# Optimization experiments

Hardware: AMD Instinct MI355X
Metric: run time of the kernel (lower is better)

## Reference

```python
import jax, jax.numpy as jnp
import numpy as np

B, TK, NK, H = 64, 512, 256, 512

def _masked_renorm_softmax(scores, mask):
    # softmax over last dim, multiply by mask, renormalize (as in the torch code)
    p = jax.nn.softmax(scores, axis=-1) * mask
    return p / jnp.sum(p, axis=-1, keepdims=True)

def setup_inputs() -> dict:
    key = jax.random.key(0)
    ks = jax.random.split(key, 14)
    s = 0.02
    return {
        "s_t_hat": jax.random.normal(ks[0], (B, 2 * H), jnp.float32),
        "encoder_outputs_token": jax.random.normal(ks[1], (B, TK, H), jnp.float32),
        "encoder_outputs_node": jax.random.normal(ks[2], (B, NK, H), jnp.float32),
        "node_to_token": jax.random.randint(ks[3], (B, TK), 0, NK),
        "enc_padding_mask_token": jnp.ones((B, TK), jnp.float32),
        "enc_padding_mask_node": jnp.ones((B, NK), jnp.float32),
        "graph": jax.random.uniform(ks[4], (B, NK, NK), jnp.float32),
        "flow": jax.random.uniform(ks[5], (B, NK), jnp.float32),
        # parameters (Linear weights stored as [in, out]; x @ W == torch Linear)
        "W_c": jax.random.normal(ks[6], (H,), jnp.float32) * s,          # Linear(1, H)
        "W_tok": jax.random.normal(ks[7], (H, H), jnp.float32) * s,      # encode_proj_token
        "W_node": jax.random.normal(ks[8], (H, H), jnp.float32) * s,     # encode_proj_node
        "W_dec": jax.random.normal(ks[9], (2 * H, H), jnp.float32) * s,  # decode_proj
        "b_dec": jnp.zeros((H,), jnp.float32),
        "v_tok": jax.random.normal(ks[10], (H,), jnp.float32) * s,       # v_token
        "v_node": jax.random.normal(ks[11], (H,), jnp.float32) * s,      # v_node
    }

def reference(s_t_hat, encoder_outputs_token, encoder_outputs_node, node_to_token,
              enc_padding_mask_token, enc_padding_mask_node, graph, flow,
              W_c, W_tok, W_node, W_dec, b_dec, v_tok, v_node):
    # projections
    enc_tok_feat = jnp.einsum('bth,hk->btk', encoder_outputs_token, W_tok)   # [B,TK,H]
    enc_node_feat = jnp.einsum('bnh,hk->bnk', encoder_outputs_node, W_node)  # [B,NK,H]
    dec_fea = s_t_hat @ W_dec + b_dec                                        # [B,H]
    flow_feat = flow[..., None] * W_c                                        # [B,NK,H]

    # node attention
    e_node = jnp.tanh(enc_node_feat + dec_fea[:, None, :] + flow_feat)
    scores_node = jnp.einsum('bnh,h->bn', e_node, v_node)                    # [B,NK]
    attn_dist_node = _masked_renorm_softmax(scores_node, enc_padding_mask_node)

    # gather node attention onto tokens via node_to_token indices
    gathered = jnp.take_along_axis(attn_dist_node, node_to_token, axis=1)    # [B,TK]
    attn_dist_node_to_token = _masked_renorm_softmax(gathered, enc_padding_mask_token)

    # token attention
    e_tok = jnp.tanh(enc_tok_feat + dec_fea[:, None, :])
    scores_tok = jnp.einsum('bth,h->bt', e_tok, v_tok)                       # [B,TK]
    attn_dist_token = _masked_renorm_softmax(scores_tok, enc_padding_mask_token)

    # mix and context
    final_attn = 0.5 * attn_dist_token + 0.5 * attn_dist_node_to_token      # [B,TK]
    c_t = jnp.einsum('bt,bth->bh', final_attn, encoder_outputs_token)        # [B,H]

    # multi-hop graph diffusion of node attention
    zero_hop = attn_dist_node                                                # [B,NK]
    one_hop = jnp.einsum('bn,bnm->bm', zero_hop, graph)
    two_hop = jnp.einsum('bn,bnm->bm', one_hop, graph)
    flow_out = (zero_hop + one_hop + two_hop) * 0.33333

    return (c_t, final_attn, attn_dist_node, flow_out)
```

## Files before the change

### kernel.cpp

```cpp
#include <hip/hip_runtime.h>
#include <math.h>

constexpr int kB = 64;
constexpr int kTK = 512;
constexpr int kNK = 256;
constexpr int kH = 512;
constexpr int kTokBlocks = kB * kTK / 64;
constexpr int kNodeBlocks = kB * kNK / 64;

typedef float f32x4 __attribute__((ext_vector_type(4)));
typedef __bf16 bf16x8 __attribute__((ext_vector_type(8)));
typedef unsigned short u16x8 __attribute__((ext_vector_type(8)));

__device__ __forceinline__ unsigned short f32_to_bf16(float f) {
  return (unsigned short)((__float_as_uint(f) + 0x8000u) >> 16);
}

__device__ __forceinline__ float tanh_fast(float x) {
  float e = __builtin_amdgcn_exp2f(x * 2.8853900817779268f);
  return 1.0f - 2.0f * __builtin_amdgcn_rcpf(e + 1.0f);
}

__device__ __forceinline__ void lds_barrier() {
  __builtin_amdgcn_s_waitcnt(0xC07F);
  __builtin_amdgcn_s_barrier();
}

__global__ __launch_bounds__(256) void prep_kernel(
    const float* __restrict__ Wtok, const float* __restrict__ Wnode,
    unsigned short* __restrict__ WtokT, unsigned short* __restrict__ WnodeT,
    const float* __restrict__ s_t_hat, const float* __restrict__ W_dec,
    float* __restrict__ dec_part) {
  __shared__ float sm[32 * 33];
  const int tid = threadIdx.x;
  if (blockIdx.x < 512) {
    const int idx = blockIdx.x;
    const int z = idx >> 8, rem = idx & 255;
    const int bx = rem & 15, by = rem >> 4;
    const float* W = z ? Wnode : Wtok;
    unsigned short* T = z ? WnodeT : WtokT;
    const int tx = tid & 31, ty = tid >> 5;
#pragma unroll
    for (int i = 0; i < 4; ++i)
      sm[(ty + 8 * i) * 33 + tx] =
          W[(size_t)(by * 32 + ty + 8 * i) * kH + bx * 32 + tx];
    __syncthreads();
#pragma unroll
    for (int i = 0; i < 4; ++i)
      T[(size_t)(bx * 32 + ty + 8 * i) * kH + by * 32 + tx] =
          f32_to_bf16(sm[tx * 33 + ty + 8 * i]);
  } else {
    const int r = blockIdx.x - 512;
    const int b = r >> 3, s = r & 7;
    if (tid < 128) sm[tid] = s_t_hat[(size_t)b * 1024 + s * 128 + tid];
    __syncthreads();
    float a0 = 0.f, a1 = 0.f;
    const float* w = W_dec + (size_t)(s * 128) * kH;
#pragma unroll 8
    for (int k = 0; k < 128; ++k) {
      a0 = fmaf(sm[k], w[(size_t)k * kH + tid], a0);
      a1 = fmaf(sm[k], w[(size_t)k * kH + tid + 256], a1);
    }
    dec_part[(size_t)(b * 8 + s) * kH + tid] = a0;
    dec_part[(size_t)(b * 8 + s) * kH + tid + 256] = a1;
  }
}

__global__ __launch_bounds__(1024, 4) void scores_fused_kernel(
    const float* __restrict__ enc_tok, const float* __restrict__ enc_node,
    const unsigned short* __restrict__ WtokT,
    const unsigned short* __restrict__ WnodeT,
    const float* __restrict__ dec_part, const float* __restrict__ b_dec,
    const float* __restrict__ flow, const float* __restrict__ W_c,
    const float* __restrict__ v_tok, const float* __restrict__ v_node,
    float* __restrict__ scores_tok, float* __restrict__ scores_node) {
  const int tid = threadIdx.x;
  const int wave = tid >> 6, lane = tid & 63;
  const int quad = lane >> 4, l15 = lane & 15;
  const bool is_node = blockIdx.x >= kTokBlocks;
  const int bidx = is_node ? (int)blockIdx.x - kTokBlocks : (int)blockIdx.x;
  const float* A = is_node ? enc_node : enc_tok;
  const unsigned short* WT = is_node ? WnodeT : WtokT;
  const float* v = is_node ? v_node : v_tok;
  float* scores = is_node ? scores_node : scores_tok;
  const int ROWS = is_node ? kNK : kTK;
  const int b = is_node ? (bidx >> 2) : (bidx >> 3);
  const int row0 = (is_node ? (bidx & 3) : (bidx & 7)) * 64;

  __shared__ __align__(16) unsigned short As[2][8192];
  __shared__ float red[16][64];

  const f32x4 fzero = {0.f, 0.f, 0.f, 0.f};
  f32x4 acc[4][2];
#pragma unroll
  for (int i = 0; i < 4; ++i)
#pragma unroll
    for (int j = 0; j < 2; ++j) acc[i][j] = fzero;

  const int arow = ((tid >> 6) & 3) * 16 + (tid & 15);
  const int akk = (tid >> 8) * 32 + ((tid >> 4) & 3) * 8;
  const float* aptr = A + (size_t)(b * ROWS + row0 + arow) * kH + akk;
  float4 ax0, ax1;
  auto aload = [&](int kc) {
    ax0 = *(const float4*)(aptr + kc * 128);
    ax1 = *(const float4*)(aptr + kc * 128 + 4);
  };
  auto acommit = [&](int buf) {
    u16x8 h;
    h[0] = f32_to_bf16(ax0.x); h[1] = f32_to_bf16(ax0.y);
    h[2] = f32_to_bf16(ax0.z); h[3] = f32_to_bf16(ax0.w);
    h[4] = f32_to_bf16(ax1.x); h[5] = f32_to_bf16(ax1.y);
    h[6] = f32_to_bf16(ax1.z); h[7] = f32_to_bf16(ax1.w);
    *(u16x8*)&As[buf][tid * 8] = h;
  };

  const int n0 = wave * 32;
  const unsigned short* bbase = WT + (size_t)(n0 + l15) * kH + quad * 8;
  bf16x8 bbuf[2][2];
  auto loadB = [&](int sb, int g) {
    bbuf[sb][0] = *(const bf16x8*)(bbase + g * 32);
    bbuf[sb][1] = *(const bf16x8*)(bbase + (size_t)16 * kH + g * 32);
  };

  aload(0);
  acommit(0);
  aload(1);
  loadB(0, 0);
  lds_barrier();

#pragma unroll
  for (int g = 0; g < 16; ++g) {
    const int kc = g >> 2, kh = g & 3;
    if (kh == 0 && kc < 3) {
      acommit((kc + 1) & 1);
      if (kc < 2) aload(kc + 2);
    }
    if (g < 15) loadB((g + 1) & 1, g + 1);
    bf16x8 afr[4];
#pragma unroll
    for (int mi = 0; mi < 4; ++mi)
      afr[mi] = *(const bf16x8*)&As[kc & 1][((kh * 4 + mi) * 64 + lane) * 8];
#pragma unroll
    for (int mi = 0; mi < 4; ++mi)
#pragma unroll
      for (int ni = 0; ni < 2; ++ni)
        acc[mi][ni] = __builtin_amdgcn_mfma_f32_16x16x32_bf16(
            afr[mi], bbuf[g & 1][ni], acc[mi][ni], 0, 0, 0);
    if (kh == 3 && kc < 3) lds_barrier();
  }

  float dec2[2], vv2[2], wc2[2];
#pragma unroll
  for (int ni = 0; ni < 2; ++ni) {
    const int col = n0 + 16 * ni + l15;
    float d = b_dec[col];
#pragma unroll
    for (int p = 0; p < 8; ++p) d += dec_part[(size_t)(b * 8 + p) * kH + col];
    dec2[ni] = d;
    vv2[ni] = v[col];
    wc2[ni] = is_node ? W_c[col] : 0.f;
  }
#pragma unroll
  for (int mi = 0; mi < 4; ++mi) {
#pragma unroll
    for (int reg = 0; reg < 4; ++reg) {
      const int row = 16 * mi + quad * 4 + reg;
      const float fl = is_node ? flow[b * kNK + row0 + row] : 0.f;
      float p = 0.f;
#pragma unroll
      for (int ni = 0; ni < 2; ++ni)
        p += tanh_fast(fmaf(fl, wc2[ni], acc[mi][ni][reg] + dec2[ni])) * vv2[ni];
#pragma unroll
      for (int off = 1; off < 16; off <<= 1) p += __shfl_xor(p, off, 64);
      if (l15 == 0) red[wave][row] = p;
    }
  }
  __syncthreads();
  if (tid < 64) {
    float s = 0.f;
#pragma unroll
    for (int w = 0; w < 16; ++w) s += red[w][tid];
    scores[b * ROWS + row0 + tid] = s;
  }
}

__device__ __forceinline__ float block_sum_512(float v, float* rbuf) {
#pragma unroll
  for (int off = 32; off >= 1; off >>= 1) v += __shfl_xor(v, off, 64);
  if ((threadIdx.x & 63) == 0) rbuf[threadIdx.x >> 6] = v;
  __syncthreads();
  float s = rbuf[0];
#pragma unroll
  for (int w = 1; w < 8; ++w) s += rbuf[w];
  __syncthreads();
  return s;
}

__global__ __launch_bounds__(512) void softmax_mix_kernel(
    const float* __restrict__ scores_node, const float* __restrict__ scores_tok,
    const int* __restrict__ node_to_token,
    const float* __restrict__ mask_tok, const float* __restrict__ mask_node,
    float* __restrict__ out_final, float* __restrict__ out_attn_node,
    float* __restrict__ out_flow) {
  const int b = blockIdx.x, tid = threadIdx.x;
  __shared__ float an_sh[kNK];
  __shared__ float rbuf[8];

  if (tid < kNK) out_flow[b * kNK + tid] = 0.f;

  float en = 0.f;
  if (tid < kNK)
    en = expf(scores_node[b * kNK + tid]) * mask_node[b * kNK + tid];
  float sn = block_sum_512(en, rbuf);
  float an = en / sn;
  if (tid < kNK) {
    an_sh[tid] = an;
    out_attn_node[b * kNK + tid] = an;
  }
  __syncthreads();

  const float mt = mask_tok[b * kTK + tid];
  const int idx = node_to_token[b * kTK + tid];
  float eg = expf(an_sh[idx]) * mt;
  float sg = block_sum_512(eg, rbuf);
  float an2t = eg / sg;

  float et = expf(scores_tok[b * kTK + tid]) * mt;
  float st = block_sum_512(et, rbuf);
  float at = et / st;

  out_final[b * kTK + tid] = 0.5f * (at + an2t);
}

__global__ __launch_bounds__(512) void ct_flow1_kernel(
    const float* __restrict__ final_attn, const float* __restrict__ enc_tok,
    const float* __restrict__ attn_node, const float* __restrict__ graph,
    float* __restrict__ ctp, float* __restrict__ fp1) {
  __shared__ float sm[64];
  const int tid = threadIdx.x;
  if (blockIdx.x < 512) {
    const int s = blockIdx.x & 7, b = blockIdx.x >> 3;
    if (tid < 64) sm[tid] = final_attn[b * kTK + s * 64 + tid];
    __syncthreads();
    float acc = 0.f;
    const float* base = enc_tok + ((size_t)(b * kTK + s * 64)) * kH + tid;
#pragma unroll 16
    for (int t = 0; t < 64; ++t) acc = fmaf(sm[t], base[(size_t)t * kH], acc);
    ctp[(size_t)(b * 8 + s) * kH + tid] = acc;
  } else {
    const int r = blockIdx.x - 512;
    const int b = r >> 2, sl = r & 3;
    const int m = tid & 255, half = tid >> 8;
    if (tid < 64) sm[tid] = attn_node[b * kNK + sl * 64 + tid];
    __syncthreads();
    float acc = 0.f;
    const float* g =
        graph + ((size_t)(b * kNK + sl * 64 + half * 32)) * kNK + m;
#pragma unroll 8
    for (int n = 0; n < 32; ++n)
      acc = fmaf(sm[half * 32 + n], g[(size_t)n * kNK], acc);
    fp1[(size_t)(b * 8 + sl * 2 + half) * kNK + m] = acc;
  }
}

__global__ __launch_bounds__(512) void ct_flow2_kernel(
    const float* __restrict__ ctp, const float* __restrict__ fp1,
    const float* __restrict__ attn_node, const float* __restrict__ graph,
    float* __restrict__ out_ct, float* __restrict__ out_flow) {
  __shared__ float one_sh[64];
  const int tid = threadIdx.x;
  if (blockIdx.x < 64) {
    const int b = blockIdx.x;
    float acc = 0.f;
#pragma unroll
    for (int p = 0; p < 8; ++p) acc += ctp[(size_t)(b * 8 + p) * kH + tid];
    out_ct[b * kH + tid] = acc;
  } else {
    const int r = blockIdx.x - 64;
    const int b = r >> 2, sl = r & 3;
    const int m = tid & 255, half = tid >> 8;
    if (tid < 64) {
      const int n = sl * 64 + tid;
      float one = 0.f;
#pragma unroll
      for (int p = 0; p < 8; ++p) one += fp1[(size_t)(b * 8 + p) * kNK + n];
      one_sh[tid] = one;
      atomicAdd(&out_flow[b * kNK + n],
                (attn_node[b * kNK + n] + one) * 0.33333f);
    }
    __syncthreads();
    float acc = 0.f;
    const float* g =
        graph + ((size_t)(b * kNK + sl * 64 + half * 32)) * kNK + m;
#pragma unroll 8
    for (int n = 0; n < 32; ++n)
      acc = fmaf(one_sh[half * 32 + n], g[(size_t)n * kNK], acc);
    atomicAdd(&out_flow[b * kNK + m], acc * 0.33333f);
  }
}

extern "C" void kernel_launch(void* const* d_in, const int* in_sizes, int n_in,
                              void* d_out, int out_size, void* d_ws, size_t ws_size,
                              hipStream_t stream) {
  (void)in_sizes; (void)n_in; (void)out_size; (void)ws_size;
  const float* s_t_hat  = (const float*)d_in[0];
  const float* enc_tok  = (const float*)d_in[1];
  const float* enc_node = (const float*)d_in[2];
  const int*   n2t      = (const int*)d_in[3];
  const float* mask_tok = (const float*)d_in[4];
  const float* mask_nd  = (const float*)d_in[5];
  const float* graph    = (const float*)d_in[6];
  const float* flow     = (const float*)d_in[7];
  const float* W_c      = (const float*)d_in[8];
  const float* W_tok    = (const float*)d_in[9];
  const float* W_node   = (const float*)d_in[10];
  const float* W_dec    = (const float*)d_in[11];
  const float* b_dec    = (const float*)d_in[12];
  const float* v_tok    = (const float*)d_in[13];
  const float* v_node   = (const float*)d_in[14];

  float* out = (float*)d_out;
  float* out_ct        = out;
  float* out_final     = out + kB * kH;
  float* out_attn_node = out + 2 * kB * kH;
  float* out_flow      = out_attn_node + kB * kNK;

  float* ws = (float*)d_ws;
  float* scores_tok  = ws;
  float* scores_node = ws + 32768;
  float* dec_part    = ws + 49152;
  float* ctp         = dec_part;
  float* fp1         = ws + 311296;
  unsigned short* WtokT  = (unsigned short*)(ws + 442368);
  unsigned short* WnodeT = WtokT + kH * kH;

  prep_kernel<<<1024, 256, 0, stream>>>(W_tok, W_node, WtokT, WnodeT,
                                        s_t_hat, W_dec, dec_part);
  scores_fused_kernel<<<kTokBlocks + kNodeBlocks, 1024, 0, stream>>>(
      enc_tok, enc_node, WtokT, WnodeT, dec_part, b_dec, flow, W_c,
      v_tok, v_node, scores_tok, scores_node);
  softmax_mix_kernel<<<kB, 512, 0, stream>>>(scores_node, scores_tok, n2t,
                                             mask_tok, mask_nd, out_final,
                                             out_attn_node, out_flow);
  ct_flow1_kernel<<<768, 512, 0, stream>>>(out_final, enc_tok, out_attn_node,
                                           graph, ctp, fp1);
  ct_flow2_kernel<<<320, 512, 0, stream>>>(ctp, fp1, out_attn_node, graph,
                                           out_ct, out_flow);
}
```

Measured before the change: 243.7 us.

## Coalesce A-tile loads and vectorize context and graph diffusion kernels

The A-tile staging in the fused scores kernel now has each thread read contiguous float4 chunks along a row, then scatters the bf16 results into the same fragment layout in LDS with computed addresses. This replaces strided global loads that were arranged to match the MFMA fragment order. The context-vector and graph-hop kernels switch to float4 loads with fewer blocks, each covering more tokens or nodes, and reduce partial sums in shared memory. This cuts the number of partials and atomics but lowers block-level parallelism for the context reduction.

```diff
diff --git a/kernel.cpp b/kernel.cpp
--- a/kernel.cpp
+++ b/kernel.cpp
@@ -10,7 +10,6 @@
 
 typedef float f32x4 __attribute__((ext_vector_type(4)));
 typedef __bf16 bf16x8 __attribute__((ext_vector_type(8)));
-typedef unsigned short u16x8 __attribute__((ext_vector_type(8)));
 
 __device__ __forceinline__ unsigned short f32_to_bf16(float f) {
   return (unsigned short)((__float_as_uint(f) + 0x8000u) >> 16);
@@ -97,21 +96,28 @@
 #pragma unroll
     for (int j = 0; j < 2; ++j) acc[i][j] = fzero;
 
-  const int arow = ((tid >> 6) & 3) * 16 + (tid & 15);
-  const int akk = (tid >> 8) * 32 + ((tid >> 4) & 3) * 8;
-  const float* aptr = A + (size_t)(b * ROWS + row0 + arow) * kH + akk;
+  const int r = tid >> 4;
+  const int kcol = tid & 15;
+  const float* aptr = A + (size_t)(b * ROWS + row0 + r) * kH + kcol * 4;
+  const int k0 = kcol * 4;
+  const int k1 = 64 + kcol * 4;
+  const int addr0 = (((k0 >> 5) * 4 + (r >> 4)) * 64 + ((k0 >> 3) & 3) * 16 +
+                     (r & 15)) * 8 + (k0 & 7);
+  const int addr1 = (((k1 >> 5) * 4 + (r >> 4)) * 64 + ((k1 >> 3) & 3) * 16 +
+                     (r & 15)) * 8 + (k1 & 7);
   float4 ax0, ax1;
   auto aload = [&](int kc) {
     ax0 = *(const float4*)(aptr + kc * 128);
-    ax1 = *(const float4*)(aptr + kc * 128 + 4);
+    ax1 = *(const float4*)(aptr + kc * 128 + 64);
   };
   auto acommit = [&](int buf) {
-    u16x8 h;
-    h[0] = f32_to_bf16(ax0.x); h[1] = f32_to_bf16(ax0.y);
-    h[2] = f32_to_bf16(ax0.z); h[3] = f32_to_bf16(ax0.w);
-    h[4] = f32_to_bf16(ax1.x); h[5] = f32_to_bf16(ax1.y);
-    h[6] = f32_to_bf16(ax1.z); h[7] = f32_to_bf16(ax1.w);
-    *(u16x8*)&As[buf][tid * 8] = h;
+    ushort4 h0, h1;
+    h0.x = f32_to_bf16(ax0.x); h0.y = f32_to_bf16(ax0.y);
+    h0.z = f32_to_bf16(ax0.z); h0.w = f32_to_bf16(ax0.w);
+    h1.x = f32_to_bf16(ax1.x); h1.y = f32_to_bf16(ax1.y);
+    h1.z = f32_to_bf16(ax1.z); h1.w = f32_to_bf16(ax1.w);
+    *(ushort4*)&As[buf][addr0] = h0;
+    *(ushort4*)&As[buf][addr1] = h1;
   };
 
   const int n0 = wave * 32;
@@ -236,30 +242,53 @@
     const float* __restrict__ final_attn, const float* __restrict__ enc_tok,
     const float* __restrict__ attn_node, const float* __restrict__ graph,
     float* __restrict__ ctp, float* __restrict__ fp1) {
-  __shared__ float sm[64];
   const int tid = threadIdx.x;
-  if (blockIdx.x < 512) {
-    const int s = blockIdx.x & 7, b = blockIdx.x >> 3;
-    if (tid < 64) sm[tid] = final_attn[b * kTK + s * 64 + tid];
-    __syncthreads();
-    float acc = 0.f;
-    const float* base = enc_tok + ((size_t)(b * kTK + s * 64)) * kH + tid;
-#pragma unroll 16
-    for (int t = 0; t < 64; ++t) acc = fmaf(sm[t], base[(size_t)t * kH], acc);
-    ctp[(size_t)(b * 8 + s) * kH + tid] = acc;
+  if (blockIdx.x < 128) {
+    const int b = blockIdx.x >> 1, s = blockIdx.x & 1;
+    __shared__ float fa[256];
+    if (tid < 256) fa[tid] = final_attn[b * kTK + s * 256 + tid];
+    __syncthreads();
+    const int h4 = (tid & 127) * 4, tsub = tid >> 7;
+    float4 acc = {0.f, 0.f, 0.f, 0.f};
+    const float* base =
+        enc_tok + ((size_t)(b * kTK + s * 256 + tsub * 64)) * kH + h4;
+#pragma unroll 8
+    for (int t = 0; t < 64; ++t) {
+      float4 e = *(const float4*)(base + (size_t)t * kH);
+      const float w = fa[tsub * 64 + t];
+      acc.x = fmaf(w, e.x, acc.x); acc.y = fmaf(w, e.y, acc.y);
+      acc.z = fmaf(w, e.z, acc.z); acc.w = fmaf(w, e.w, acc.w);
+    }
+    *(float4*)&ctp[((size_t)(b * 8 + s * 4 + tsub)) * kH + h4] = acc;
   } else {
-    const int r = blockIdx.x - 512;
-    const int b = r >> 2, sl = r & 3;
-    const int m = tid & 255, half = tid >> 8;
-    if (tid < 64) sm[tid] = attn_node[b * kNK + sl * 64 + tid];
-    __syncthreads();
-    float acc = 0.f;
+    const int rr = blockIdx.x - 128;
+    const int b = rr >> 2, sl = rr & 3;
+    __shared__ float z[64];
+    __shared__ float part[8][256];
+    if (tid < 64) z[tid] = attn_node[b * kNK + sl * 64 + tid];
+    __syncthreads();
+    const int m4 = (tid & 63) * 4, nsub = tid >> 6;
+    float4 acc = {0.f, 0.f, 0.f, 0.f};
     const float* g =
-        graph + ((size_t)(b * kNK + sl * 64 + half * 32)) * kNK + m;
-#pragma unroll 8
-    for (int n = 0; n < 32; ++n)
-      acc = fmaf(sm[half * 32 + n], g[(size_t)n * kNK], acc);
-    fp1[(size_t)(b * 8 + sl * 2 + half) * kNK + m] = acc;
+        graph + ((size_t)(b * kNK + sl * 64 + nsub * 8)) * kNK + m4;
+#pragma unroll
+    for (int n = 0; n < 8; ++n) {
+      float4 gg = *(const float4*)(g + (size_t)n * kNK);
+      const float w = z[nsub * 8 + n];
+      acc.x = fmaf(w, gg.x, acc.x); acc.y = fmaf(w, gg.y, acc.y);
+      acc.z = fmaf(w, gg.z, acc.z); acc.w = fmaf(w, gg.w, acc.w);
+    }
+    *(float4*)&part[nsub][m4] = acc;
+    __syncthreads();
+    if (tid < 64) {
+      float4 s0 = {0.f, 0.f, 0.f, 0.f};
+#pragma unroll
+      for (int p = 0; p < 8; ++p) {
+        float4 pp = *(const float4*)&part[p][tid * 4];
+        s0.x += pp.x; s0.y += pp.y; s0.z += pp.z; s0.w += pp.w;
+      }
+      *(float4*)&fp1[((size_t)(b * 4 + sl)) * kNK + tid * 4] = s0;
+    }
   }
 }
 
@@ -267,35 +296,69 @@
     const float* __restrict__ ctp, const float* __restrict__ fp1,
     const float* __restrict__ attn_node, const float* __restrict__ graph,
     float* __restrict__ out_ct, float* __restrict__ out_flow) {
-  __shared__ float one_sh[64];
   const int tid = threadIdx.x;
   if (blockIdx.x < 64) {
     const int b = blockIdx.x;
-    float acc = 0.f;
-#pragma unroll
-    for (int p = 0; p < 8; ++p) acc += ctp[(size_t)(b * 8 + p) * kH + tid];
-    out_ct[b * kH + tid] = acc;
+    __shared__ float acc_sh[4][512];
+    const int h4 = (tid & 127) * 4, part = tid >> 7;
+    float4 a = {0.f, 0.f, 0.f, 0.f};
+#pragma unroll
+    for (int j = 0; j < 2; ++j) {
+      float4 c = *(const float4*)&ctp[((size_t)(b * 8 + part * 2 + j)) * kH + h4];
+      a.x += c.x; a.y += c.y; a.z += c.z; a.w += c.w;
+    }
+    *(float4*)&acc_sh[part][h4] = a;
+    __syncthreads();
+    if (tid < 128) {
+      float4 s = {0.f, 0.f, 0.f, 0.f};
+#pragma unroll
+      for (int p = 0; p < 4; ++p) {
+        float4 pp = *(const float4*)&acc_sh[p][tid * 4];
+        s.x += pp.x; s.y += pp.y; s.z += pp.z; s.w += pp.w;
+      }
+      *(float4*)&out_ct[b * kH + tid * 4] = s;
+    }
   } else {
-    const int r = blockIdx.x - 64;
-    const int b = r >> 2, sl = r & 3;
-    const int m = tid & 255, half = tid >> 8;
+    const int rr = blockIdx.x - 64;
+    const int b = rr >> 2, sl = rr & 3;
+    __shared__ float one_sh[64];
+    __shared__ float part2[8][256];
     if (tid < 64) {
       const int n = sl * 64 + tid;
       float one = 0.f;
 #pragma unroll
-      for (int p = 0; p < 8; ++p) one += fp1[(size_t)(b * 8 + p) * kNK + n];
+      for (int p = 0; p < 4; ++p) one += fp1[((size_t)(b * 4 + p)) * kNK + n];
       one_sh[tid] = one;
       atomicAdd(&out_flow[b * kNK + n],
                 (attn_node[b * kNK + n] + one) * 0.33333f);
     }
     __syncthreads();
-    float acc = 0.f;
+    const int m4 = (tid & 63) * 4, nsub = tid >> 6;
+    float4 acc = {0.f, 0.f, 0.f, 0.f};
     const float* g =
-        graph + ((size_t)(b * kNK + sl * 64 + half * 32)) * kNK + m;
-#pragma unroll 8
-    for (int n = 0; n < 32; ++n)
-      acc = fmaf(one_sh[half * 32 + n], g[(size_t)n * kNK], acc);
-    atomicAdd(&out_flow[b * kNK + m], acc * 0.33333f);
+        graph + ((size_t)(b * kNK + sl * 64 + nsub * 8)) * kNK + m4;
+#pragma unroll
+    for (int n = 0; n < 8; ++n) {
+      float4 gg = *(const float4*)(g + (size_t)n * kNK);
+      const float w = one_sh[sl * 0 + nsub * 8 + n];
+      acc.x = fmaf(w, gg.x, acc.x); acc.y = fmaf(w, gg.y, acc.y);
+      acc.z = fmaf(w, gg.z, acc.z); acc.w = fmaf(w, gg.w, acc.w);
+    }
+    *(float4*)&part2[nsub][m4] = acc;
+    __syncthreads();
+    if (tid < 64) {
+      float4 s = {0.f, 0.f, 0.f, 0.f};
+#pragma unroll
+      for (int p = 0; p < 8; ++p) {
+        float4 pp = *(const float4*)&part2[p][tid * 4];
+        s.x += pp.x; s.y += pp.y; s.z += pp.z; s.w += pp.w;
+      }
+      float* dst = &out_flow[b * kNK + tid * 4];
+      atomicAdd(dst + 0, s.x * 0.33333f);
+      atomicAdd(dst + 1, s.y * 0.33333f);
+      atomicAdd(dst + 2, s.z * 0.33333f);
+      atomicAdd(dst + 3, s.w * 0.33333f);
+    }
   }
 }
 
@@ -331,7 +394,7 @@
   float* dec_part    = ws + 49152;
   float* ctp         = dec_part;
   float* fp1         = ws + 311296;
-  unsigned short* WtokT  = (unsigned short*)(ws + 442368);
+  unsigned short* WtokT  = (unsigned short*)(ws + 376832);
   unsigned short* WnodeT = WtokT + kH * kH;
 
   prep_kernel<<<1024, 256, 0, stream>>>(W_tok, W_node, WtokT, WnodeT,
@@ -342,7 +405,7 @@
   softmax_mix_kernel<<<kB, 512, 0, stream>>>(scores_node, scores_tok, n2t,
                                              mask_tok, mask_nd, out_final,
                                              out_attn_node, out_flow);
-  ct_flow1_kernel<<<768, 512, 0, stream>>>(out_final, enc_tok, out_attn_node,
+  ct_flow1_kernel<<<384, 512, 0, stream>>>(out_final, enc_tok, out_attn_node,
                                            graph, ctp, fp1);
   ct_flow2_kernel<<<320, 512, 0, stream>>>(ctp, fp1, out_attn_node, graph,
                                            out_ct, out_flow);
```

Result: no change. 241.8 us (-0.8%).
